# Optimization experiments

Hardware: AMD Instinct MI355X
Metric: run time of the kernel (lower is better)

Reference implementation:

```python
import jax, jax.numpy as jnp
import numpy as np

# Dims fixed by ExpertC.__init__ defaults
INPUT_DIM, HIDDEN, OUT_DIM, NLAYERS = 1024, 256, 256, 2
D_STATE, EXPAND, HEADDIM = 32, 2, 32
D_INNER = EXPAND * HIDDEN                      # 512
NHEADS = D_INNER // HEADDIM                    # 16
CONV_DIM = D_INNER + 2 * D_STATE               # 576 (x, B, C; ngroups=1)
D_IN_PROJ = 2 * D_INNER + 2 * D_STATE + NHEADS # 1104 (z, xBC, dt)
KCONV = 4
B, L = 16, 2048
EPS = 1e-5


def setup_inputs() -> dict:
    key = jax.random.key(0)
    ks = iter(jax.random.split(key, 40))
    rn = lambda shape, s: jax.random.normal(next(ks), shape, jnp.float32) * s
    inp = {}
    inp["x"] = rn((B, L, INPUT_DIM), 1.0)
    inp["ip_w"] = rn((INPUT_DIM, HIDDEN), INPUT_DIM ** -0.5)
    inp["ip_b"] = jnp.zeros((HIDDEN,), jnp.float32)
    inp["m_inw"] = rn((NLAYERS, HIDDEN, D_IN_PROJ), HIDDEN ** -0.5)
    inp["m_inb"] = jnp.zeros((NLAYERS, D_IN_PROJ), jnp.float32)
    inp["m_convw"] = rn((NLAYERS, CONV_DIM, KCONV), 0.3)
    inp["m_convb"] = jnp.zeros((NLAYERS, CONV_DIM), jnp.float32)
    inp["m_dtb"] = rn((NLAYERS, NHEADS), 0.5)
    inp["m_Alog"] = jnp.log(1.0 + 15.0 * jax.random.uniform(next(ks), (NLAYERS, NHEADS), jnp.float32))
    inp["m_D"] = jnp.ones((NLAYERS, NHEADS), jnp.float32)
    inp["m_nw"] = jnp.ones((NLAYERS, D_INNER), jnp.float32)
    inp["m_outw"] = rn((NLAYERS, D_INNER, HIDDEN), D_INNER ** -0.5)
    inp["m_outb"] = jnp.zeros((NLAYERS, HIDDEN), jnp.float32)
    inp["rms_w"] = jnp.ones((NLAYERS, HIDDEN), jnp.float32)
    inp["ln1_w"] = jnp.ones((HIDDEN,), jnp.float32)
    inp["ln1_b"] = jnp.zeros((HIDDEN,), jnp.float32)
    inp["w1"] = rn((HIDDEN, 2 * HIDDEN), HIDDEN ** -0.5)
    inp["b1"] = jnp.zeros((2 * HIDDEN,), jnp.float32)
    inp["w2"] = rn((2 * HIDDEN, OUT_DIM), (2 * HIDDEN) ** -0.5)
    inp["b2"] = jnp.zeros((OUT_DIM,), jnp.float32)
    inp["ln2_w"] = jnp.ones((OUT_DIM,), jnp.float32)
    inp["ln2_b"] = jnp.zeros((OUT_DIM,), jnp.float32)
    return inp


def rmsnorm(x, w):
    return x * jax.lax.rsqrt(jnp.mean(x * x, axis=-1, keepdims=True) + EPS) * w


def layernorm(x, w, b):
    m = jnp.mean(x, axis=-1, keepdims=True)
    v = jnp.mean((x - m) ** 2, axis=-1, keepdims=True)
    return (x - m) * jax.lax.rsqrt(v + EPS) * w + b


def mamba_layer(x, inw, inb, convw, convb, dtb, Alog, D, nw, outw, outb):
    b, l, _ = x.shape
    zxbcdt = x @ inw + inb                                   # (b,l,1104)
    z, xBC, dt = jnp.split(zxbcdt, [D_INNER, D_INNER + CONV_DIM], axis=-1)
    dt = jax.nn.softplus(dt + dtb)                           # (b,l,h)
    # causal depthwise conv1d (kernel 4) + silu
    xp = jnp.pad(xBC, ((0, 0), (KCONV - 1, 0), (0, 0)))
    xBC = sum(xp[:, i:i + l, :] * convw[:, i] for i in range(KCONV)) + convb
    xBC = jax.nn.silu(xBC)
    xs, Bm, Cm = jnp.split(xBC, [D_INNER, D_INNER + D_STATE], axis=-1)
    xh = xs.reshape(b, l, NHEADS, HEADDIM)                   # (b,l,h,p)
    A = -jnp.exp(Alog)                                       # (h,)
    dA = jnp.exp(dt * A)                                     # (b,l,h)
    dtx = dt[..., None] * xh                                 # (b,l,h,p)

    def step(h, inp):
        dA_t, dtx_t, B_t, C_t = inp
        # h: (b,h,p,n)
        h = h * dA_t[:, :, None, None] + dtx_t[..., None] * B_t[:, None, None, :]
        y = jnp.einsum('bhpn,bn->bhp', h, C_t)
        return h, y

    h0 = jnp.zeros((b, NHEADS, HEADDIM, D_STATE), x.dtype)
    xs_t = (jnp.moveaxis(dA, 1, 0), jnp.moveaxis(dtx, 1, 0),
            jnp.moveaxis(Bm, 1, 0), jnp.moveaxis(Cm, 1, 0))
    _, ys = jax.lax.scan(step, h0, xs_t)                     # (l,b,h,p)
    y = jnp.moveaxis(ys, 0, 1) + D[None, None, :, None] * xh
    y = y.reshape(b, l, D_INNER)
    y = rmsnorm(y * jax.nn.silu(z), nw)                      # gated RMSNorm
    return y @ outw + outb


def _expert(x, ip_w, ip_b, m_inw, m_inb, m_convw, m_convb, m_dtb, m_Alog, m_D,
            m_nw, m_outw, m_outb, rms_w, ln1_w, ln1_b, w1, b1, w2, b2, ln2_w, ln2_b):
    if x.ndim == 2:
        x = x[:, None, :]
    x = x @ ip_w + ip_b
    for i in range(NLAYERS):
        res = x
        x = mamba_layer(x, m_inw[i], m_inb[i], m_convw[i], m_convb[i], m_dtb[i],
                        m_Alog[i], m_D[i], m_nw[i], m_outw[i], m_outb[i])
        x = rmsnorm(x + res, rms_w[i])
    x = layernorm(x, ln1_w, ln1_b)
    x = jax.nn.gelu(x @ w1 + b1, approximate=False)          # dropout is eval no-op
    x = x @ w2 + b2
    return layernorm(x, ln2_w, ln2_b)


def reference(x, ip_w, ip_b, m_inw, m_inb, m_convw, m_convb, m_dtb, m_Alog, m_D,
              m_nw, m_outw, m_outb, rms_w, ln1_w, ln1_b, w1, b1, w2, b2, ln2_w, ln2_b):
    return _expert(x, ip_w, ip_b, m_inw, m_inb, m_convw, m_convb, m_dtb, m_Alog, m_D,
                   m_nw, m_outw, m_outb, rms_w, ln1_w, ln1_b, w1, b1, w2, b2, ln2_w, ln2_b)
```

## Files before the change

### kernel.cpp

```cpp
#include <hip/hip_runtime.h>

typedef __bf16 bf16;
typedef __bf16 bf16x8 __attribute__((ext_vector_type(8)));
typedef float  f32x4  __attribute__((ext_vector_type(4)));

#define EPSF 1e-5f

__device__ __forceinline__ float bf2f(bf16 x) { return (float)x; }
__device__ __forceinline__ bf16  f2bf(float x) { return (bf16)x; }
__device__ __forceinline__ float siluf(float x) { return x / (1.f + expf(-x)); }

__global__ __launch_bounds__(256) void gemm_split(
    const float* __restrict__ A, int lda,
    const float* __restrict__ W, int ldw,
    const float* __restrict__ bias,
    int N, int K,
    float* __restrict__ outF, int ldF,
    bf16* __restrict__ outB, int ldB,
    int doGelu)
{
    __shared__ bf16 As [128][40];
    __shared__ bf16 Als[128][40];
    __shared__ bf16 Bs [64][40];
    __shared__ bf16 Bls[64][40];

    const int tid  = threadIdx.x;
    const int lane = tid & 63;
    const int wid  = tid >> 6;
    const int waveM = wid & 1, waveN = wid >> 1;
    const int m16 = lane & 15, quad = lane >> 4;
    const int row0 = blockIdx.x * 128;
    const int n0   = blockIdx.y * 64;

    f32x4 acc[4][2];
#pragma unroll
    for (int i = 0; i < 4; ++i)
#pragma unroll
        for (int j = 0; j < 2; ++j)
            acc[i][j] = (f32x4){0.f, 0.f, 0.f, 0.f};

    const int ar = tid >> 1, akc = (tid & 1) * 16;
    const int bn = tid & 63, bk0 = tid >> 6;
    const bool nok = (n0 + bn) < N;

    for (int k0 = 0; k0 < K; k0 += 32) {
        {
            const float* asrc = A + (size_t)(row0 + ar) * lda + k0 + akc;
            bf16* dh = &As [ar][akc];
            bf16* dl = &Als[ar][akc];
#pragma unroll
            for (int c = 0; c < 4; ++c) {
                float4 f = ((const float4*)asrc)[c];
#pragma unroll
                for (int e = 0; e < 4; ++e) {
                    float v = (&f.x)[e];
                    bf16 hi = f2bf(v);
                    dh[c * 4 + e] = hi;
                    dl[c * 4 + e] = f2bf(v - bf2f(hi));
                }
            }
        }
        {
            const float* wsrc = W + (size_t)k0 * ldw + n0 + bn;
#pragma unroll
            for (int it = 0; it < 8; ++it) {
                int k_l = bk0 + it * 4;
                float v = 0.f;
                if (nok) v = wsrc[(size_t)k_l * ldw];
                bf16 hi = f2bf(v);
                Bs [bn][k_l] = hi;
                Bls[bn][k_l] = f2bf(v - bf2f(hi));
            }
        }
        __syncthreads();

        bf16x8 aH[4], aL[4], bH[2], bL[2];
#pragma unroll
        for (int mi = 0; mi < 4; ++mi) {
            aH[mi] = *(const bf16x8*)&As [waveM * 64 + mi * 16 + m16][quad * 8];
            aL[mi] = *(const bf16x8*)&Als[waveM * 64 + mi * 16 + m16][quad * 8];
        }
#pragma unroll
        for (int ni = 0; ni < 2; ++ni) {
            bH[ni] = *(const bf16x8*)&Bs [waveN * 32 + ni * 16 + m16][quad * 8];
            bL[ni] = *(const bf16x8*)&Bls[waveN * 32 + ni * 16 + m16][quad * 8];
        }

#pragma unroll
        for (int mi = 0; mi < 4; ++mi)
#pragma unroll
            for (int ni = 0; ni < 2; ++ni) {
                acc[mi][ni] = __builtin_amdgcn_mfma_f32_16x16x32_bf16(
                    aH[mi], bH[ni], acc[mi][ni], 0, 0, 0);
                acc[mi][ni] = __builtin_amdgcn_mfma_f32_16x16x32_bf16(
                    aH[mi], bL[ni], acc[mi][ni], 0, 0, 0);
                acc[mi][ni] = __builtin_amdgcn_mfma_f32_16x16x32_bf16(
                    aL[mi], bH[ni], acc[mi][ni], 0, 0, 0);
            }
        __syncthreads();
    }

#pragma unroll
    for (int ni = 0; ni < 2; ++ni) {
        int col = n0 + waveN * 32 + ni * 16 + m16;
        if (col >= N) continue;
        float bv = bias ? bias[col] : 0.f;
#pragma unroll
        for (int mi = 0; mi < 4; ++mi) {
#pragma unroll
            for (int r = 0; r < 4; ++r) {
                int row = row0 + waveM * 64 + mi * 16 + quad * 4 + r;
                float v = acc[mi][ni][r] + bv;
                if (doGelu) v = 0.5f * v * (1.f + erff(v * 0.70710678118654752f));
                if (outB) outB[(size_t)row * ldB + col] = f2bf(v);
                if (outF) outF[(size_t)row * ldF + col] = v;
            }
        }
    }
}

__global__ __launch_bounds__(192) void conv_kernel(
    const bf16* __restrict__ zx,
    const float* __restrict__ cw,
    const float* __restrict__ cb,
    float* __restrict__ xs,
    float* __restrict__ Bc,
    float* __restrict__ Cc)
{
    int row = blockIdx.x;
    int ch  = blockIdx.y * 192 + threadIdx.x;
    int l   = row & 2047;
    float acc = cb[ch];
#pragma unroll
    for (int i = 0; i < 4; ++i) {
        int ls = l + i - 3;
        if (ls >= 0)
            acc += bf2f(zx[(size_t)(row + i - 3) * 1104 + 512 + ch]) * cw[ch * 4 + i];
    }
    float s = siluf(acc);
    if (ch < 512)      xs[(size_t)row * 512 + ch]        = s;
    else if (ch < 544) Bc[(size_t)row * 32 + (ch - 512)] = s;
    else               Cc[(size_t)row * 32 + (ch - 544)] = s;
}

__global__ __launch_bounds__(256) void dtproj_kernel(
    const float* __restrict__ h,
    const float* __restrict__ inw,
    const float* __restrict__ inb,
    const float* __restrict__ dtbp,
    const float* __restrict__ Alog,
    float* __restrict__ dtf,
    float* __restrict__ dAf)
{
    __shared__ float wl[256][16];
    __shared__ float hl[256];
    __shared__ float red[16][17];
    int tid = threadIdx.x;
    int row = blockIdx.x;

    {
        const float* src = inw + (size_t)tid * 1104 + 1088;
        *(float4*)&wl[tid][0]  = ((const float4*)src)[0];
        *(float4*)&wl[tid][4]  = ((const float4*)src)[1];
        *(float4*)&wl[tid][8]  = ((const float4*)src)[2];
        *(float4*)&wl[tid][12] = ((const float4*)src)[3];
    }
    if (tid < 64)
        *(float4*)&hl[tid * 4] = *(const float4*)(h + (size_t)row * 256 + tid * 4);
    __syncthreads();

    int hh = tid >> 4, g = tid & 15;
    float s = 0.f;
#pragma unroll
    for (int i = 0; i < 16; ++i) {
        int k = g * 16 + i;
        s += hl[k] * wl[k][hh];
    }
    red[hh][g] = s;
    __syncthreads();

    if (tid < 16) {
        float tot = inb[1088 + tid];
#pragma unroll
        for (int i = 0; i < 16; ++i) tot += red[tid][i];
        float xx = tot + dtbp[tid];
        float sp = (xx > 20.f) ? xx : log1pf(expf(xx));
        float A  = -expf(Alog[tid]);
        dtf[(size_t)row * 16 + tid] = sp;
        dAf[(size_t)row * 16 + tid] = expf(sp * A);
    }
}

#define QCH   256
#define NCH   8

struct StepB  { float Bv[16]; float da, dtv, xv; };
struct StepBC { float Bv[16]; float Cv[16]; float da, dtv, xv; };

__device__ __forceinline__ void load_stepB(
    StepB& S, const float* Bc, const float* dtf, const float* dAf,
    const float* xs, size_t r, int h, int p, int nb)
{
    const float4* bp = (const float4*)(Bc + r * 32 + nb);
    *(float4*)&S.Bv[0]  = bp[0];
    *(float4*)&S.Bv[4]  = bp[1];
    *(float4*)&S.Bv[8]  = bp[2];
    *(float4*)&S.Bv[12] = bp[3];
    S.da  = dAf[r * 16 + h];
    S.dtv = dtf[r * 16 + h];
    S.xv  = xs[r * 512 + h * 32 + p];
}

__device__ __forceinline__ void load_stepBC(
    StepBC& S, const float* Bc, const float* Cc, const float* dtf,
    const float* dAf, const float* xs, size_t r, int h, int p, int nb)
{
    const float4* bp = (const float4*)(Bc + r * 32 + nb);
    *(float4*)&S.Bv[0]  = bp[0];
    *(float4*)&S.Bv[4]  = bp[1];
    *(float4*)&S.Bv[8]  = bp[2];
    *(float4*)&S.Bv[12] = bp[3];
    const float4* cp = (const float4*)(Cc + r * 32 + nb);
    *(float4*)&S.Cv[0]  = cp[0];
    *(float4*)&S.Cv[4]  = cp[1];
    *(float4*)&S.Cv[8]  = cp[2];
    *(float4*)&S.Cv[12] = cp[3];
    S.da  = dAf[r * 16 + h];
    S.dtv = dtf[r * 16 + h];
    S.xv  = xs[r * 512 + h * 32 + p];
}

__global__ __launch_bounds__(64) void scan_phase1(
    const float* __restrict__ xs,
    const float* __restrict__ Bc,
    const float* __restrict__ dtf,
    const float* __restrict__ dAf,
    float* __restrict__ cs,
    float* __restrict__ cp)
{
    int blk = blockIdx.x;
    int bh = blk >> 3, c = blk & (NCH - 1);
    int b = bh >> 4, h = bh & 15;
    int lane = threadIdx.x;
    int p = lane & 31, half = lane >> 5, nb = half * 16;
    float hs[16];
#pragma unroll
    for (int j = 0; j < 16; ++j) hs[j] = 0.f;
    float P = 1.f;
    size_t rb = (size_t)b * 2048 + (size_t)c * QCH;

    StepB S0, S1;
    load_stepB(S0, Bc, dtf, dAf, xs, rb, h, p, nb);

    for (int t = 0; t < QCH; t += 2) {
        load_stepB(S1, Bc, dtf, dAf, xs, rb + t + 1, h, p, nb);
        {
            float dtx = S0.dtv * S0.xv, da = S0.da;
#pragma unroll
            for (int j = 0; j < 16; ++j)
                hs[j] = fmaf(hs[j], da, dtx * S0.Bv[j]);
            P *= da;
        }
        if (t + 2 < QCH)
            load_stepB(S0, Bc, dtf, dAf, xs, rb + t + 2, h, p, nb);
        {
            float dtx = S1.dtv * S1.xv, da = S1.da;
#pragma unroll
            for (int j = 0; j < 16; ++j)
                hs[j] = fmaf(hs[j], da, dtx * S1.Bv[j]);
            P *= da;
        }
    }

    float* dst = cs + (size_t)blk * 1024 + lane * 16;
#pragma unroll
    for (int q = 0; q < 4; ++q)
        ((float4*)dst)[q] = (float4){hs[q*4], hs[q*4+1], hs[q*4+2], hs[q*4+3]};
    if (lane == 0) cp[blk] = P;
}

__global__ __launch_bounds__(64) void scan_phase2(
    float* __restrict__ cs,
    const float* __restrict__ cp)
{
    int bh = blockIdx.x;
    int lane = threadIdx.x;
    float H[16];
#pragma unroll
    for (int j = 0; j < 16; ++j) H[j] = 0.f;
    for (int c = 0; c < NCH; ++c) {
        float* base = cs + ((size_t)(bh * NCH + c)) * 1024 + lane * 16;
        float E[16];
#pragma unroll
        for (int q = 0; q < 4; ++q) {
            float4 v = ((const float4*)base)[q];
            E[q*4] = v.x; E[q*4+1] = v.y; E[q*4+2] = v.z; E[q*4+3] = v.w;
        }
        float P = cp[bh * NCH + c];
#pragma unroll
        for (int q = 0; q < 4; ++q)
            ((float4*)base)[q] = (float4){H[q*4], H[q*4+1], H[q*4+2], H[q*4+3]};
#pragma unroll
        for (int j = 0; j < 16; ++j)
            H[j] = fmaf(H[j], P, E[j]);
    }
}

__global__ __launch_bounds__(64) void scan_phase3(
    const float* __restrict__ xs,
    const float* __restrict__ Bc,
    const float* __restrict__ Cc,
    const float* __restrict__ dtf,
    const float* __restrict__ dAf,
    const float* __restrict__ Dv,
    const float* __restrict__ cs,
    bf16* __restrict__ y)
{
    int blk = blockIdx.x;
    int bh = blk >> 3, c = blk & (NCH - 1);
    int b = bh >> 4, h = bh & 15;
    int lane = threadIdx.x;
    int p = lane & 31, half = lane >> 5, nb = half * 16;
    float Dh = Dv[h];
    float hs[16];
    {
        const float* src = cs + (size_t)blk * 1024 + lane * 16;
#pragma unroll
        for (int q = 0; q < 4; ++q) {
            float4 v = ((const float4*)src)[q];
            hs[q*4] = v.x; hs[q*4+1] = v.y; hs[q*4+2] = v.z; hs[q*4+3] = v.w;
        }
    }
    size_t rb = (size_t)b * 2048 + (size_t)c * QCH;

    StepBC S0, S1;
    load_stepBC(S0, Bc, Cc, dtf, dAf, xs, rb, h, p, nb);

    for (int t = 0; t < QCH; t += 2) {
        load_stepBC(S1, Bc, Cc, dtf, dAf, xs, rb + t + 1, h, p, nb);
        {
            float dtx = S0.dtv * S0.xv, da = S0.da, yv = 0.f;
#pragma unroll
            for (int j = 0; j < 16; ++j) {
                hs[j] = fmaf(hs[j], da, dtx * S0.Bv[j]);
                yv = fmaf(hs[j], S0.Cv[j], yv);
            }
            yv += __shfl_xor(yv, 32);
            if (half == 0)
                y[(rb + t) * 512 + h * 32 + p] = f2bf(yv + Dh * S0.xv);
        }
        if (t + 2 < QCH)
            load_stepBC(S0, Bc, Cc, dtf, dAf, xs, rb + t + 2, h, p, nb);
        {
            float dtx = S1.dtv * S1.xv, da = S1.da, yv = 0.f;
#pragma unroll
            for (int j = 0; j < 16; ++j) {
                hs[j] = fmaf(hs[j], da, dtx * S1.Bv[j]);
                yv = fmaf(hs[j], S1.Cv[j], yv);
            }
            yv += __shfl_xor(yv, 32);
            if (half == 0)
                y[(rb + t + 1) * 512 + h * 32 + p] = f2bf(yv + Dh * S1.xv);
        }
    }
}

__global__ __launch_bounds__(64) void gaterms_kernel(
    const bf16* __restrict__ y,
    const bf16* __restrict__ zx,
    const float* __restrict__ nw,
    float* __restrict__ outp)
{
    int row = blockIdx.x, lane = threadIdx.x;
    union { uint4 u; bf16 b[8]; } yv, zv;
    yv.u = *(const uint4*)(y  + (size_t)row * 512  + lane * 8);
    zv.u = *(const uint4*)(zx + (size_t)row * 1104 + lane * 8);
    float4 nv0 = *(const float4*)(nw + lane * 8);
    float4 nv1 = *(const float4*)(nw + lane * 8 + 4);
    float nvv[8] = {nv0.x, nv0.y, nv0.z, nv0.w, nv1.x, nv1.y, nv1.z, nv1.w};
    float g[8]; float ss = 0.f;
#pragma unroll
    for (int i = 0; i < 8; ++i) {
        float gate = siluf(bf2f(zv.b[i]));
        g[i] = bf2f(yv.b[i]) * gate;
        ss += g[i] * g[i];
    }
#pragma unroll
    for (int o = 1; o < 64; o <<= 1) ss += __shfl_xor(ss, o);
    float rms = rsqrtf(ss * (1.f / 512.f) + EPSF);
    float* op = outp + (size_t)row * 512 + lane * 8;
    ((float4*)op)[0] = (float4){g[0]*rms*nvv[0], g[1]*rms*nvv[1], g[2]*rms*nvv[2], g[3]*rms*nvv[3]};
    ((float4*)op)[1] = (float4){g[4]*rms*nvv[4], g[5]*rms*nvv[5], g[6]*rms*nvv[6], g[7]*rms*nvv[7]};
}

__global__ __launch_bounds__(64) void resrms_kernel(
    const float* __restrict__ mo,
    float* __restrict__ h,
    const float* __restrict__ w)
{
    int row = blockIdx.x, lane = threadIdx.x;
    float4 a = *(const float4*)(mo + (size_t)row * 256 + lane * 4);
    float4 r = *(const float4*)(h  + (size_t)row * 256 + lane * 4);
    float s0 = a.x + r.x, s1 = a.y + r.y, s2 = a.z + r.z, s3 = a.w + r.w;
    float ss = s0 * s0 + s1 * s1 + s2 * s2 + s3 * s3;
#pragma unroll
    for (int o = 1; o < 64; o <<= 1) ss += __shfl_xor(ss, o);
    float rms = rsqrtf(ss * (1.f / 256.f) + EPSF);
    float4 wv = *(const float4*)(w + lane * 4);
    *(float4*)(h + (size_t)row * 256 + lane * 4) =
        (float4){s0 * rms * wv.x, s1 * rms * wv.y, s2 * rms * wv.z, s3 * rms * wv.w};
}

__global__ __launch_bounds__(64) void ln_kernel(
    const float* __restrict__ x,
    const float* __restrict__ w,
    const float* __restrict__ b,
    float* __restrict__ outp)
{
    int row = blockIdx.x, lane = threadIdx.x;
    float4 v = *(const float4*)(x + (size_t)row * 256 + lane * 4);
    float sum = v.x + v.y + v.z + v.w;
    float sq  = v.x * v.x + v.y * v.y + v.z * v.z + v.w * v.w;
#pragma unroll
    for (int o = 1; o < 64; o <<= 1) { sum += __shfl_xor(sum, o); sq += __shfl_xor(sq, o); }
    float m  = sum * (1.f / 256.f);
    float var = sq * (1.f / 256.f) - m * m;
    float is = rsqrtf(var + EPSF);
    float4 wv = *(const float4*)(w + lane * 4);
    float4 bv = *(const float4*)(b + lane * 4);
    *(float4*)(outp + (size_t)row * 256 + lane * 4) = (float4){
        (v.x - m) * is * wv.x + bv.x,
        (v.y - m) * is * wv.y + bv.y,
        (v.z - m) * is * wv.z + bv.z,
        (v.w - m) * is * wv.w + bv.w};
}

extern "C" void kernel_launch(void* const* d_in, const int* in_sizes, int n_in,
                              void* d_out, int out_size, void* d_ws, size_t ws_size,
                              hipStream_t stream)
{
    const float* x      = (const float*)d_in[0];
    const float* ip_w   = (const float*)d_in[1];
    const float* ip_b   = (const float*)d_in[2];
    const float* m_inw  = (const float*)d_in[3];
    const float* m_inb  = (const float*)d_in[4];
    const float* m_convw= (const float*)d_in[5];
    const float* m_convb= (const float*)d_in[6];
    const float* m_dtb  = (const float*)d_in[7];
    const float* m_Alog = (const float*)d_in[8];
    const float* m_D    = (const float*)d_in[9];
    const float* m_nw   = (const float*)d_in[10];
    const float* m_outw = (const float*)d_in[11];
    const float* m_outb = (const float*)d_in[12];
    const float* rms_w  = (const float*)d_in[13];
    const float* ln1_w  = (const float*)d_in[14];
    const float* ln1_b  = (const float*)d_in[15];
    const float* w1     = (const float*)d_in[16];
    const float* b1     = (const float*)d_in[17];
    const float* w2     = (const float*)d_in[18];
    const float* b2     = (const float*)d_in[19];
    const float* ln2_w  = (const float*)d_in[20];
    const float* ln2_b  = (const float*)d_in[21];

    const int M = 32768;
    char* wsb = (char*)d_ws;
    size_t off = 0;
    auto alloc = [&](size_t bytes) {
        void* p = wsb + off;
        off += (bytes + 255) & ~(size_t)255;
        return p;
    };
    bf16*  zx   = (bf16*) alloc((size_t)M * 1104 * 2);
    float* h    = (float*)alloc((size_t)M * 256 * 4);
    float* U1   = (float*)alloc((size_t)M * 512 * 4);
    float* Bc   = (float*)alloc((size_t)M * 32 * 4);
    float* Cc   = (float*)alloc((size_t)M * 32 * 4);
    float* dtf  = (float*)alloc((size_t)M * 16 * 4);
    float* dAf  = (float*)alloc((size_t)M * 16 * 4);
    bf16*  ybuf = (bf16*) alloc((size_t)M * 512 * 2);
    float* cs   = (float*)alloc((size_t)2048 * 1024 * 4);
    float* cpb  = (float*)alloc((size_t)2048 * 4);
    (void)ws_size; (void)in_sizes; (void)n_in; (void)out_size;

    float* xs     = U1;
    float* normed = U1;
    float* tb     = U1;
    float* mo     = (float*)zx;
    float* gbuf   = (float*)zx;
    float* ubuf   = (float*)ybuf;

    dim3 blk(256);

    gemm_split<<<dim3(256, 4), blk, 0, stream>>>(
        x, 1024, ip_w, 256, ip_b, 256, 1024, h, 256, nullptr, 0, 0);

    for (int L = 0; L < 2; ++L) {
        const float* inw = m_inw  + (size_t)L * 256 * 1104;
        const float* inb = m_inb  + (size_t)L * 1104;
        const float* cw  = m_convw+ (size_t)L * 576 * 4;
        const float* cb  = m_convb+ (size_t)L * 576;
        const float* dtb = m_dtb  + L * 16;
        const float* Al  = m_Alog + L * 16;
        const float* Dv  = m_D    + L * 16;
        const float* nw  = m_nw   + (size_t)L * 512;
        const float* ow  = m_outw + (size_t)L * 512 * 256;
        const float* ob  = m_outb + (size_t)L * 256;
        const float* rw  = rms_w  + (size_t)L * 256;

        gemm_split<<<dim3(256, 18), blk, 0, stream>>>(
            h, 256, inw, 1104, inb, 1104, 256, nullptr, 0, zx, 1104, 0);
        conv_kernel<<<dim3(M, 3), 192, 0, stream>>>(zx, cw, cb, xs, Bc, Cc);
        dtproj_kernel<<<M, 256, 0, stream>>>(h, inw, inb, dtb, Al, dtf, dAf);
        scan_phase1<<<2048, 64, 0, stream>>>(xs, Bc, dtf, dAf, cs, cpb);
        scan_phase2<<<256, 64, 0, stream>>>(cs, cpb);
        scan_phase3<<<2048, 64, 0, stream>>>(xs, Bc, Cc, dtf, dAf, Dv, cs, ybuf);
        gaterms_kernel<<<M, 64, 0, stream>>>(ybuf, zx, nw, normed);
        gemm_split<<<dim3(256, 4), blk, 0, stream>>>(
            normed, 512, ow, 256, ob, 256, 512, mo, 256, nullptr, 0, 0);
        resrms_kernel<<<M, 64, 0, stream>>>(mo, h, rw);
    }

    ln_kernel<<<M, 64, 0, stream>>>(h, ln1_w, ln1_b, tb);
    gemm_split<<<dim3(256, 8), blk, 0, stream>>>(
        tb, 256, w1, 512, b1, 512, 256, gbuf, 512, nullptr, 0, 1);
    gemm_split<<<dim3(256, 4), blk, 0, stream>>>(
        gbuf, 512, w2, 256, b2, 256, 512, ubuf, 256, nullptr, 0, 0);
    ln_kernel<<<M, 64, 0, stream>>>(ubuf, ln2_w, ln2_b, (float*)d_out);
}
```

Before: 1.874 ms.

## Prepack weights as transposed bf16 hi/lo splits and fuse dt projection into in-proj GEMM

Adds a prepack kernel that converts every weight matrix once per call into transposed bf16 hi/lo pairs. The GEMM then reads B fragments directly from global memory with register double-buffering instead of splitting and staging them in shared memory. Producer kernels (gated RMSNorm, LayerNorm, GELU GEMM) now emit hi/lo bf16 activations, so the next GEMM skips its fp32 split, and the dt softplus/exp epilogue is folded into the in-projection GEMM, removing the separate dtproj kernel. The cost is an extra prepack launch and uncoalesced per-lane global B loads.

```diff
diff --git a/kernel.cpp b/kernel.cpp
--- a/kernel.cpp
+++ b/kernel.cpp
@@ -10,19 +10,42 @@
 __device__ __forceinline__ bf16  f2bf(float x) { return (bf16)x; }
 __device__ __forceinline__ float siluf(float x) { return x / (1.f + expf(-x)); }
 
-__global__ __launch_bounds__(256) void gemm_split(
-    const float* __restrict__ A, int lda,
-    const float* __restrict__ W, int ldw,
+struct PrepackArgs {
+    const float* W[7];
+    bf16* TH[7];
+    bf16* TL[7];
+    int K[7];
+    int N[7];
+};
+
+__global__ __launch_bounds__(256) void prepack_kernel(PrepackArgs a)
+{
+    int s = blockIdx.y;
+    int idx = blockIdx.x * 256 + threadIdx.x;
+    int K = a.K[s], N = a.N[s];
+    if (idx >= K * N) return;
+    int k = idx / N, n = idx - k * N;
+    float v = a.W[s][idx];
+    bf16 hi = f2bf(v);
+    a.TH[s][(size_t)n * K + k] = hi;
+    a.TL[s][(size_t)n * K + k] = f2bf(v - bf2f(hi));
+}
+
+__global__ __launch_bounds__(256) void gemm_hl(
+    const bf16* __restrict__ AH, const bf16* __restrict__ AL,
+    const float* __restrict__ Af, int lda,
+    const bf16* __restrict__ WTh, const bf16* __restrict__ WTl,
     const float* __restrict__ bias,
     int N, int K,
     float* __restrict__ outF, int ldF,
     bf16* __restrict__ outB, int ldB,
-    int doGelu)
+    bf16* __restrict__ outH, bf16* __restrict__ outL, int ldH,
+    int doGelu,
+    const float* __restrict__ dtb, const float* __restrict__ Alog,
+    float* __restrict__ dtf, float* __restrict__ dAf)
 {
     __shared__ bf16 As [128][40];
     __shared__ bf16 Als[128][40];
-    __shared__ bf16 Bs [64][40];
-    __shared__ bf16 Bls[64][40];
 
     const int tid  = threadIdx.x;
     const int lane = tid & 63;
@@ -40,12 +63,30 @@
             acc[i][j] = (f32x4){0.f, 0.f, 0.f, 0.f};
 
     const int ar = tid >> 1, akc = (tid & 1) * 16;
-    const int bn = tid & 63, bk0 = tid >> 6;
-    const bool nok = (n0 + bn) < N;
+
+    const int bn0 = min(n0 + waveN * 32 + m16,      N - 1);
+    const int bn1 = min(n0 + waveN * 32 + 16 + m16, N - 1);
+    const bf16* bH0p = WTh + (size_t)bn0 * K + quad * 8;
+    const bf16* bH1p = WTh + (size_t)bn1 * K + quad * 8;
+    const bf16* bL0p = WTl + (size_t)bn0 * K + quad * 8;
+    const bf16* bL1p = WTl + (size_t)bn1 * K + quad * 8;
+
+    bf16x8 bH[2], bL[2], bHn[2], bLn[2];
+    bH[0] = *(const bf16x8*)(bH0p);
+    bH[1] = *(const bf16x8*)(bH1p);
+    bL[0] = *(const bf16x8*)(bL0p);
+    bL[1] = *(const bf16x8*)(bL1p);
 
     for (int k0 = 0; k0 < K; k0 += 32) {
-        {
-            const float* asrc = A + (size_t)(row0 + ar) * lda + k0 + akc;
+        if (AH) {
+            const bf16* s0 = AH + (size_t)(row0 + ar) * lda + k0 + akc;
+            const bf16* s1 = AL + (size_t)(row0 + ar) * lda + k0 + akc;
+            *(uint4*)&As [ar][akc]     = *(const uint4*)s0;
+            *(uint4*)&As [ar][akc + 8] = *(const uint4*)(s0 + 8);
+            *(uint4*)&Als[ar][akc]     = *(const uint4*)s1;
+            *(uint4*)&Als[ar][akc + 8] = *(const uint4*)(s1 + 8);
+        } else {
+            const float* asrc = Af + (size_t)(row0 + ar) * lda + k0 + akc;
             bf16* dh = &As [ar][akc];
             bf16* dl = &Als[ar][akc];
 #pragma unroll
@@ -60,30 +101,22 @@
                 }
             }
         }
-        {
-            const float* wsrc = W + (size_t)k0 * ldw + n0 + bn;
-#pragma unroll
-            for (int it = 0; it < 8; ++it) {
-                int k_l = bk0 + it * 4;
-                float v = 0.f;
-                if (nok) v = wsrc[(size_t)k_l * ldw];
-                bf16 hi = f2bf(v);
-                Bs [bn][k_l] = hi;
-                Bls[bn][k_l] = f2bf(v - bf2f(hi));
-            }
-        }
         __syncthreads();
 
-        bf16x8 aH[4], aL[4], bH[2], bL[2];
+        const bool more = (k0 + 32) < K;
+        if (more) {
+            int kn = k0 + 32;
+            bHn[0] = *(const bf16x8*)(bH0p + kn);
+            bHn[1] = *(const bf16x8*)(bH1p + kn);
+            bLn[0] = *(const bf16x8*)(bL0p + kn);
+            bLn[1] = *(const bf16x8*)(bL1p + kn);
+        }
+
+        bf16x8 aH[4], aL[4];
 #pragma unroll
         for (int mi = 0; mi < 4; ++mi) {
             aH[mi] = *(const bf16x8*)&As [waveM * 64 + mi * 16 + m16][quad * 8];
             aL[mi] = *(const bf16x8*)&Als[waveM * 64 + mi * 16 + m16][quad * 8];
-        }
-#pragma unroll
-        for (int ni = 0; ni < 2; ++ni) {
-            bH[ni] = *(const bf16x8*)&Bs [waveN * 32 + ni * 16 + m16][quad * 8];
-            bL[ni] = *(const bf16x8*)&Bls[waveN * 32 + ni * 16 + m16][quad * 8];
         }
 
 #pragma unroll
@@ -98,6 +131,11 @@
                     aL[mi], bH[ni], acc[mi][ni], 0, 0, 0);
             }
         __syncthreads();
+
+        if (more) {
+            bH[0] = bHn[0]; bH[1] = bHn[1];
+            bL[0] = bLn[0]; bL[1] = bLn[1];
+        }
     }
 
 #pragma unroll
@@ -111,9 +149,23 @@
             for (int r = 0; r < 4; ++r) {
                 int row = row0 + waveM * 64 + mi * 16 + quad * 4 + r;
                 float v = acc[mi][ni][r] + bv;
-                if (doGelu) v = 0.5f * v * (1.f + erff(v * 0.70710678118654752f));
-                if (outB) outB[(size_t)row * ldB + col] = f2bf(v);
-                if (outF) outF[(size_t)row * ldF + col] = v;
+                if (dtf && col >= 1088) {
+                    int head = col - 1088;
+                    float xx = v + dtb[head];
+                    float sp = (xx > 20.f) ? xx : log1pf(expf(xx));
+                    float A  = -expf(Alog[head]);
+                    dtf[(size_t)row * 16 + head] = sp;
+                    dAf[(size_t)row * 16 + head] = expf(sp * A);
+                } else {
+                    if (doGelu) v = 0.5f * v * (1.f + erff(v * 0.70710678118654752f));
+                    if (outB) outB[(size_t)row * ldB + col] = f2bf(v);
+                    if (outF) outF[(size_t)row * ldF + col] = v;
+                    if (outH) {
+                        bf16 hi = f2bf(v);
+                        outH[(size_t)row * ldH + col] = hi;
+                        outL[(size_t)row * ldH + col] = f2bf(v - bf2f(hi));
+                    }
+                }
             }
         }
     }
@@ -141,54 +193,6 @@
     if (ch < 512)      xs[(size_t)row * 512 + ch]        = s;
     else if (ch < 544) Bc[(size_t)row * 32 + (ch - 512)] = s;
     else               Cc[(size_t)row * 32 + (ch - 544)] = s;
-}
-
-__global__ __launch_bounds__(256) void dtproj_kernel(
-    const float* __restrict__ h,
-    const float* __restrict__ inw,
-    const float* __restrict__ inb,
-    const float* __restrict__ dtbp,
-    const float* __restrict__ Alog,
-    float* __restrict__ dtf,
-    float* __restrict__ dAf)
-{
-    __shared__ float wl[256][16];
-    __shared__ float hl[256];
-    __shared__ float red[16][17];
-    int tid = threadIdx.x;
-    int row = blockIdx.x;
-
-    {
-        const float* src = inw + (size_t)tid * 1104 + 1088;
-        *(float4*)&wl[tid][0]  = ((const float4*)src)[0];
-        *(float4*)&wl[tid][4]  = ((const float4*)src)[1];
-        *(float4*)&wl[tid][8]  = ((const float4*)src)[2];
-        *(float4*)&wl[tid][12] = ((const float4*)src)[3];
-    }
-    if (tid < 64)
-        *(float4*)&hl[tid * 4] = *(const float4*)(h + (size_t)row * 256 + tid * 4);
-    __syncthreads();
-
-    int hh = tid >> 4, g = tid & 15;
-    float s = 0.f;
-#pragma unroll
-    for (int i = 0; i < 16; ++i) {
-        int k = g * 16 + i;
-        s += hl[k] * wl[k][hh];
-    }
-    red[hh][g] = s;
-    __syncthreads();
-
-    if (tid < 16) {
-        float tot = inb[1088 + tid];
-#pragma unroll
-        for (int i = 0; i < 16; ++i) tot += red[tid][i];
-        float xx = tot + dtbp[tid];
-        float sp = (xx > 20.f) ? xx : log1pf(expf(xx));
-        float A  = -expf(Alog[tid]);
-        dtf[(size_t)row * 16 + tid] = sp;
-        dAf[(size_t)row * 16 + tid] = expf(sp * A);
-    }
 }
 
 #define QCH   256
@@ -369,10 +373,11 @@
     const bf16* __restrict__ y,
     const bf16* __restrict__ zx,
     const float* __restrict__ nw,
-    float* __restrict__ outp)
+    bf16* __restrict__ outH,
+    bf16* __restrict__ outL)
 {
     int row = blockIdx.x, lane = threadIdx.x;
-    union { uint4 u; bf16 b[8]; } yv, zv;
+    union { uint4 u; bf16 b[8]; } yv, zv, oh, ol;
     yv.u = *(const uint4*)(y  + (size_t)row * 512  + lane * 8);
     zv.u = *(const uint4*)(zx + (size_t)row * 1104 + lane * 8);
     float4 nv0 = *(const float4*)(nw + lane * 8);
@@ -388,9 +393,15 @@
 #pragma unroll
     for (int o = 1; o < 64; o <<= 1) ss += __shfl_xor(ss, o);
     float rms = rsqrtf(ss * (1.f / 512.f) + EPSF);
-    float* op = outp + (size_t)row * 512 + lane * 8;
-    ((float4*)op)[0] = (float4){g[0]*rms*nvv[0], g[1]*rms*nvv[1], g[2]*rms*nvv[2], g[3]*rms*nvv[3]};
-    ((float4*)op)[1] = (float4){g[4]*rms*nvv[4], g[5]*rms*nvv[5], g[6]*rms*nvv[6], g[7]*rms*nvv[7]};
+#pragma unroll
+    for (int i = 0; i < 8; ++i) {
+        float v = g[i] * rms * nvv[i];
+        bf16 hi = f2bf(v);
+        oh.b[i] = hi;
+        ol.b[i] = f2bf(v - bf2f(hi));
+    }
+    *(uint4*)(outH + (size_t)row * 512 + lane * 8) = oh.u;
+    *(uint4*)(outL + (size_t)row * 512 + lane * 8) = ol.u;
 }
 
 __global__ __launch_bounds__(64) void resrms_kernel(
@@ -415,7 +426,9 @@
     const float* __restrict__ x,
     const float* __restrict__ w,
     const float* __restrict__ b,
-    float* __restrict__ outp)
+    bf16* __restrict__ outH,
+    bf16* __restrict__ outL,
+    float* __restrict__ outF)
 {
     int row = blockIdx.x, lane = threadIdx.x;
     float4 v = *(const float4*)(x + (size_t)row * 256 + lane * 4);
@@ -428,11 +441,24 @@
     float is = rsqrtf(var + EPSF);
     float4 wv = *(const float4*)(w + lane * 4);
     float4 bv = *(const float4*)(b + lane * 4);
-    *(float4*)(outp + (size_t)row * 256 + lane * 4) = (float4){
-        (v.x - m) * is * wv.x + bv.x,
-        (v.y - m) * is * wv.y + bv.y,
-        (v.z - m) * is * wv.z + bv.z,
-        (v.w - m) * is * wv.w + bv.w};
+    float o0 = (v.x - m) * is * wv.x + bv.x;
+    float o1 = (v.y - m) * is * wv.y + bv.y;
+    float o2 = (v.z - m) * is * wv.z + bv.z;
+    float o3 = (v.w - m) * is * wv.w + bv.w;
+    if (outH) {
+        union { uint2 u; bf16 bb[4]; } oh, ol;
+        float o[4] = {o0, o1, o2, o3};
+#pragma unroll
+        for (int i = 0; i < 4; ++i) {
+            bf16 hi = f2bf(o[i]);
+            oh.bb[i] = hi;
+            ol.bb[i] = f2bf(o[i] - bf2f(hi));
+        }
+        *(uint2*)(outH + (size_t)row * 256 + lane * 4) = oh.u;
+        *(uint2*)(outL + (size_t)row * 256 + lane * 4) = ol.u;
+    }
+    if (outF)
+        *(float4*)(outF + (size_t)row * 256 + lane * 4) = (float4){o0, o1, o2, o3};
 }
 
 extern "C" void kernel_launch(void* const* d_in, const int* in_sizes, int n_in,
@@ -480,22 +506,54 @@
     bf16*  ybuf = (bf16*) alloc((size_t)M * 512 * 2);
     float* cs   = (float*)alloc((size_t)2048 * 1024 * 4);
     float* cpb  = (float*)alloc((size_t)2048 * 4);
+    bf16* ipTH   = (bf16*)alloc(262144 * 2);
+    bf16* ipTL   = (bf16*)alloc(262144 * 2);
+    bf16* inwTH0 = (bf16*)alloc(282624 * 2);
+    bf16* inwTL0 = (bf16*)alloc(282624 * 2);
+    bf16* inwTH1 = (bf16*)alloc(282624 * 2);
+    bf16* inwTL1 = (bf16*)alloc(282624 * 2);
+    bf16* outwTH0= (bf16*)alloc(131072 * 2);
+    bf16* outwTL0= (bf16*)alloc(131072 * 2);
+    bf16* outwTH1= (bf16*)alloc(131072 * 2);
+    bf16* outwTL1= (bf16*)alloc(131072 * 2);
+    bf16* w1TH   = (bf16*)alloc(131072 * 2);
+    bf16* w1TL   = (bf16*)alloc(131072 * 2);
+    bf16* w2TH   = (bf16*)alloc(131072 * 2);
+    bf16* w2TL   = (bf16*)alloc(131072 * 2);
     (void)ws_size; (void)in_sizes; (void)n_in; (void)out_size;
 
-    float* xs     = U1;
-    float* normed = U1;
-    float* tb     = U1;
-    float* mo     = (float*)zx;
-    float* gbuf   = (float*)zx;
-    float* ubuf   = (float*)ybuf;
+    float* xs      = U1;
+    bf16*  normedH = (bf16*)U1;
+    bf16*  normedL = normedH + (size_t)M * 512;
+    bf16*  tbH     = (bf16*)U1;
+    bf16*  tbL     = tbH + (size_t)M * 256;
+    float* mo      = (float*)zx;
+    bf16*  gH      = (bf16*)zx;
+    bf16*  gL      = gH + (size_t)M * 512;
+    float* ubuf    = (float*)ybuf;
+
+    PrepackArgs pa;
+    pa.W[0] = ip_w;               pa.TH[0] = ipTH;    pa.TL[0] = ipTL;    pa.K[0] = 1024; pa.N[0] = 256;
+    pa.W[1] = m_inw;              pa.TH[1] = inwTH0;  pa.TL[1] = inwTL0;  pa.K[1] = 256;  pa.N[1] = 1104;
+    pa.W[2] = m_inw + 256*1104;   pa.TH[2] = inwTH1;  pa.TL[2] = inwTL1;  pa.K[2] = 256;  pa.N[2] = 1104;
+    pa.W[3] = m_outw;             pa.TH[3] = outwTH0; pa.TL[3] = outwTL0; pa.K[3] = 512;  pa.N[3] = 256;
+    pa.W[4] = m_outw + 512*256;   pa.TH[4] = outwTH1; pa.TL[4] = outwTL1; pa.K[4] = 512;  pa.N[4] = 256;
+    pa.W[5] = w1;                 pa.TH[5] = w1TH;    pa.TL[5] = w1TL;    pa.K[5] = 256;  pa.N[5] = 512;
+    pa.W[6] = w2;                 pa.TH[6] = w2TH;    pa.TL[6] = w2TL;    pa.K[6] = 512;  pa.N[6] = 256;
+    prepack_kernel<<<dim3(1104, 7), 256, 0, stream>>>(pa);
 
     dim3 blk(256);
 
-    gemm_split<<<dim3(256, 4), blk, 0, stream>>>(
-        x, 1024, ip_w, 256, ip_b, 256, 1024, h, 256, nullptr, 0, 0);
+    gemm_hl<<<dim3(256, 4), blk, 0, stream>>>(
+        nullptr, nullptr, x, 1024, ipTH, ipTL, ip_b, 256, 1024,
+        h, 256, nullptr, 0, nullptr, nullptr, 0, 0,
+        nullptr, nullptr, nullptr, nullptr);
 
     for (int L = 0; L < 2; ++L) {
-        const float* inw = m_inw  + (size_t)L * 256 * 1104;
+        const bf16* inwTH = L ? inwTH1 : inwTH0;
+        const bf16* inwTL = L ? inwTL1 : inwTL0;
+        const bf16* outwTH= L ? outwTH1 : outwTH0;
+        const bf16* outwTL= L ? outwTL1 : outwTL0;
         const float* inb = m_inb  + (size_t)L * 1104;
         const float* cw  = m_convw+ (size_t)L * 576 * 4;
         const float* cb  = m_convb+ (size_t)L * 576;
@@ -503,27 +561,33 @@
         const float* Al  = m_Alog + L * 16;
         const float* Dv  = m_D    + L * 16;
         const float* nw  = m_nw   + (size_t)L * 512;
-        const float* ow  = m_outw + (size_t)L * 512 * 256;
         const float* ob  = m_outb + (size_t)L * 256;
         const float* rw  = rms_w  + (size_t)L * 256;
 
-        gemm_split<<<dim3(256, 18), blk, 0, stream>>>(
-            h, 256, inw, 1104, inb, 1104, 256, nullptr, 0, zx, 1104, 0);
+        gemm_hl<<<dim3(256, 18), blk, 0, stream>>>(
+            nullptr, nullptr, h, 256, inwTH, inwTL, inb, 1104, 256,
+            nullptr, 0, zx, 1104, nullptr, nullptr, 0, 0,
+            dtb, Al, dtf, dAf);
         conv_kernel<<<dim3(M, 3), 192, 0, stream>>>(zx, cw, cb, xs, Bc, Cc);
-        dtproj_kernel<<<M, 256, 0, stream>>>(h, inw, inb, dtb, Al, dtf, dAf);
         scan_phase1<<<2048, 64, 0, stream>>>(xs, Bc, dtf, dAf, cs, cpb);
         scan_phase2<<<256, 64, 0, stream>>>(cs, cpb);
         scan_phase3<<<2048, 64, 0, stream>>>(xs, Bc, Cc, dtf, dAf, Dv, cs, ybuf);
-        gaterms_kernel<<<M, 64, 0, stream>>>(ybuf, zx, nw, normed);
-        gemm_split<<<dim3(256, 4), blk, 0, stream>>>(
-            normed, 512, ow, 256, ob, 256, 512, mo, 256, nullptr, 0, 0);
+        gaterms_kernel<<<M, 64, 0, stream>>>(ybuf, zx, nw, normedH, normedL);
+        gemm_hl<<<dim3(256, 4), blk, 0, stream>>>(
+            normedH, normedL, nullptr, 512, outwTH, outwTL, ob, 256, 512,
+            mo, 256, nullptr, 0, nullptr, nullptr, 0, 0,
+            nullptr, nullptr, nullptr, nullptr);
         resrms_kernel<<<M, 64, 0, stream>>>(mo, h, rw);
     }
 
-    ln_kernel<<<M, 64, 0, stream>>>(h, ln1_w, ln1_b, tb);
-    gemm_split<<<dim3(256, 8), blk, 0, stream>>>(
-        tb, 256, w1, 512, b1, 512, 256, gbuf, 512, nullptr, 0, 1);
-    gemm_split<<<dim3(256, 4), blk, 0, stream>>>(
-        gbuf, 512, w2, 256, b2, 256, 512, ubuf, 256, nullptr, 0, 0);
-    ln_kernel<<<M, 64, 0, stream>>>(ubuf, ln2_w, ln2_b, (float*)d_out);
-}
+    ln_kernel<<<M, 64, 0, stream>>>(h, ln1_w, ln1_b, tbH, tbL, nullptr);
+    gemm_hl<<<dim3(256, 8), blk, 0, stream>>>(
+        tbH, tbL, nullptr, 256, w1TH, w1TL, b1, 512, 256,
+        nullptr, 0, nullptr, 0, gH, gL, 512, 1,
+        nullptr, nullptr, nullptr, nullptr);
+    gemm_hl<<<dim3(256, 4), blk, 0, stream>>>(
+        gH, gL, nullptr, 512, w2TH, w2TL, b2, 256, 512,
+        ubuf, 256, nullptr, 0, nullptr, nullptr, 0, 0,
+        nullptr, nullptr, nullptr, nullptr);
+    ln_kernel<<<M, 64, 0, stream>>>(ubuf, ln2_w, ln2_b, nullptr, nullptr, (float*)d_out);
+}
```

After: 1.527 ms. 1.23x faster.
